# Kernel tuning notes

Hardware: AMD Instinct MI355X
Metric: run time of the kernel (lower is better)

The kernel has to match this reference:

```python
import jax, jax.numpy as jnp
import numpy as np

CIN, HID, OUT = 128, 256, 349
NTYPES, ETYPES = 4, 5
N0, N1, N2 = 120000, 40000, 10000
GNODES, GEDGES = 250000, 2000000
E0, E1 = 1500000, 400000


def setup_inputs() -> dict:
    key = jax.random.key(0)
    ks = jax.random.split(key, 24)
    ri = jax.random.randint
    rn = jax.random.normal
    inp = {}
    inp['n_id'] = ri(ks[0], (N0,), 0, GNODES)
    inp['x0'] = rn(ks[1], (100000, CIN), dtype=jnp.float32)
    inp['src0'] = ri(ks[2], (E0,), 0, N0)
    inp['dst0'] = ri(ks[3], (E0,), 0, N1)
    inp['e_id0'] = ri(ks[4], (E0,), 0, GEDGES)
    inp['src1'] = ri(ks[5], (E1,), 0, N1)
    inp['dst1'] = ri(ks[6], (E1,), 0, N2)
    inp['e_id1'] = ri(ks[7], (E1,), 0, GEDGES)
    inp['edge_type'] = ri(ks[8], (GEDGES,), 0, ETYPES)
    inp['node_type'] = ri(ks[9], (GNODES,), 0, NTYPES)
    inp['local_node_idx'] = ri(ks[10], (GNODES,), 0, 50000)
    # learned parameters
    inp['emb1'] = rn(ks[11], (50000, CIN), dtype=jnp.float32)
    inp['emb2'] = rn(ks[12], (50000, CIN), dtype=jnp.float32)
    inp['emb3'] = rn(ks[13], (50000, CIN), dtype=jnp.float32)
    s0 = 1.0 / np.sqrt(CIN)
    s1 = 1.0 / np.sqrt(HID)
    inp['relW0'] = rn(ks[14], (ETYPES, CIN, HID), dtype=jnp.float32) * s0
    inp['rootW0'] = rn(ks[15], (NTYPES, CIN, HID), dtype=jnp.float32) * s0
    inp['rootb0'] = rn(ks[16], (NTYPES, HID), dtype=jnp.float32) * 0.02
    inp['relW1'] = rn(ks[17], (ETYPES, HID, OUT), dtype=jnp.float32) * s1
    inp['rootW1'] = rn(ks[18], (NTYPES, HID, OUT), dtype=jnp.float32) * s1
    inp['rootb1'] = rn(ks[19], (NTYPES, OUT), dtype=jnp.float32) * 0.02
    return inp


def _group_input(tables, node_type, local_node_idx, n_id):
    # RGNN.group_input: per-node-type gather from feature / embedding tables.
    nt = node_type[n_id]            # [N0]
    li = local_node_idx[n_id]       # [N0]
    h = jnp.zeros((n_id.shape[0], CIN), dtype=tables[0].dtype)
    for k, tab in enumerate(tables):
        idx = jnp.minimum(li, tab.shape[0] - 1)
        h = jnp.where((nt == k)[:, None], tab[idx], h)
    return h, nt


def _rgcn_layer(x, nt_src, src, dst, et, relW, rootW, rootb, n_tgt):
    # out = sum_t mean-aggregate(x_j over edges of type t) @ W_t  (linear commutes with mean)
    T = relW.shape[0]
    xj = x[src]                                           # [E, Cin] gather
    seg = dst * T + et                                    # fused (target, edge_type) segment id
    sums = jax.ops.segment_sum(xj, seg, num_segments=n_tgt * T)
    cnts = jax.ops.segment_sum(jnp.ones((src.shape[0],), x.dtype), seg, num_segments=n_tgt * T)
    mean = (sums / jnp.maximum(cnts, 1.0)[:, None]).reshape(n_tgt, T, -1)  # [Nt, T, Cin]
    out = jnp.einsum('ntc,tco->no', mean, relW)           # [Nt, Cout]
    # per-node-type root linear: out[mask] += root_lins[i](x_target[mask])
    x_t = x[:n_tgt]
    nt_t = nt_src[:n_tgt]
    allr = jnp.einsum('nc,tco->tno', x_t, rootW) + rootb[:, None, :]  # [Tn, Nt, Cout]
    root = jnp.take_along_axis(allr, nt_t[None, :, None], axis=0)[0]
    return out + root


def reference(n_id, x0, src0, dst0, e_id0, src1, dst1, e_id1, edge_type, node_type,
              local_node_idx, emb1, emb2, emb3, relW0, rootW0, rootb0, relW1, rootW1, rootb1):
    h, nt = _group_input([x0, emb1, emb2, emb3], node_type, local_node_idx, n_id)
    # layer 0: I -> H
    h = _rgcn_layer(h, nt, src0, dst0, edge_type[e_id0], relW0, rootW0, rootb0, N1)
    h = jax.nn.relu(h)
    nt = nt[:N1]
    # layer 1: H -> O
    h = _rgcn_layer(h, nt, src1, dst1, edge_type[e_id1], relW1, rootW1, rootb1, N2)
    return jax.nn.log_softmax(h, axis=-1)
```

## Files before the change

kernel.cpp:

```cpp
#include <hip/hip_runtime.h>
#include <hip/hip_bf16.h>
#include <cmath>

constexpr int kCIN = 128, kHID = 256, kOUT = 349;
constexpr int kNT = 4, kET = 5;
constexpr int kN0 = 120000, kN1 = 40000, kN2 = 10000;
constexpr int kNSEG0 = kN1 * kET;
constexpr int kNSEG1 = kN2 * kET;
constexpr int kNSEG = kNSEG0 + kNSEG1;

constexpr int kBinSegs = 512;
constexpr int kNBin0 = (kNSEG0 + kBinSegs - 1) / kBinSegs;
constexpr int kNBin1 = (kNSEG1 + kBinSegs - 1) / kBinSegs;
constexpr int kNBin  = kNBin0 + kNBin1;
constexpr int kNBLK  = 512;
constexpr int kSB    = 128;

typedef __bf16 bf16x8 __attribute__((ext_vector_type(8)));
typedef float f32x4 __attribute__((ext_vector_type(4)));
typedef float f32x2v __attribute__((ext_vector_type(2)));
typedef unsigned short ushort8v __attribute__((ext_vector_type(8)));

__device__ __forceinline__ unsigned short f2b(float f) {
    unsigned int b = __float_as_uint(f);
    unsigned int r = (b + 0x7FFFu + ((b >> 16) & 1u)) >> 16;
    return (unsigned short)r;
}
__device__ __forceinline__ float b2f(unsigned short u) {
    return __uint_as_float((unsigned int)u << 16);
}
__device__ __forceinline__ void gl2lds16(const void* g, void* l) {
    __builtin_amdgcn_global_load_lds(
        (const __attribute__((address_space(1))) void*)g,
        (__attribute__((address_space(3))) void*)l, 16, 0, 0);
}

__device__ __forceinline__ unsigned int f2e4m3(float f) {
#if __has_builtin(__builtin_amdgcn_cvt_pk_fp8_f32)
    return (unsigned int)(__builtin_amdgcn_cvt_pk_fp8_f32(f, f, 0, false) & 0xFF);
#else
    unsigned int sb = (__float_as_uint(f) >> 31) << 7;
    float m = fminf(fabsf(f), 448.f);
    unsigned int code;
    if (m < 0.015625f) {
        code = (unsigned int)__float2int_rn(m * 512.f);
    } else {
        unsigned int b = __float_as_uint(m);
        b = b + 0x7FFFF + ((b >> 20) & 1);
        int e8 = (int)(b >> 23) - 120;
        if (e8 > 15) code = 0x7E;
        else code = ((unsigned int)e8 << 3) | ((b >> 20) & 7);
    }
    return sb | code;
#endif
}

__device__ __forceinline__ void e4m3x4_to_f32(unsigned int u, float* o4) {
#if __has_builtin(__builtin_amdgcn_cvt_pk_f32_fp8)
    f32x2v a = __builtin_amdgcn_cvt_pk_f32_fp8(u, false);
    f32x2v b = __builtin_amdgcn_cvt_pk_f32_fp8(u, true);
    o4[0] = a[0]; o4[1] = a[1]; o4[2] = b[0]; o4[3] = b[1];
#else
#pragma unroll
    for (int i = 0; i < 4; i++) {
        unsigned int c = (u >> (8 * i)) & 0xFF;
        unsigned int s = c >> 7, e = (c >> 3) & 15, mm = c & 7;
        float v;
        if (e == 0) v = (float)mm * 0.001953125f;
        else        v = __uint_as_float((e + 120u) << 23 | mm << 20);
        o4[i] = s ? -v : v;
    }
#endif
}

__global__ void k_prep(const float* __restrict__ relW0, const float* __restrict__ rootW0,
                       unsigned short* __restrict__ Bt0T,
                       const float* __restrict__ relW1, const float* __restrict__ rootW1,
                       unsigned short* __restrict__ Bt1T,
                       const int* __restrict__ etype, unsigned char* __restrict__ et8, int nET)
{
    constexpr int T0 = kNT * 256 * 768;
    constexpr int T1 = kNT * 384 * 1536;
    constexpr int TP = T0 + T1;
    int i = blockIdx.x * 256 + threadIdx.x;
    if (i < T0) {
        int g = i / (256 * 768);
        int rem = i - g * (256 * 768);
        int col = rem / 768;
        int k = rem - col * 768;
        float v = (k < 640) ? relW0[(size_t)k * 256 + col]
                            : rootW0[((size_t)g * 128 + (k - 640)) * 256 + col];
        Bt0T[i] = f2b(v);
    } else if (i < TP) {
        int ii = i - T0;
        int g = ii / (384 * 1536);
        int rem = ii - g * (384 * 1536);
        int col = rem / 1536;
        int k = rem - col * 1536;
        float v = 0.f;
        if (col < kOUT) v = (k < 1280) ? relW1[(size_t)k * kOUT + col]
                                       : rootW1[((size_t)g * 256 + (k - 1280)) * kOUT + col];
        Bt1T[ii] = f2b(v);
    } else {
        int k = i - TP;
        if (k < nET) et8[k] = (unsigned char)etype[k];
    }
}

__global__ void k_gather(const int* __restrict__ n_id, const float* __restrict__ x0,
                         const float* __restrict__ e1, const float* __restrict__ e2,
                         const float* __restrict__ e3, const int* __restrict__ ntype,
                         const int* __restrict__ lidx, unsigned short* __restrict__ h0b,
                         unsigned char* __restrict__ h0f8, int* __restrict__ nt0)
{
    int row = blockIdx.x * 8 + (threadIdx.x >> 5);
    if (row >= kN0) return;
    int lane = threadIdx.x & 31;
    int gid = n_id[row];
    int nt = ntype[gid];
    int li = lidx[gid];
    const float* tab;
    int rows;
    if (nt == 0)      { tab = x0; rows = 100000; }
    else if (nt == 1) { tab = e1; rows = 50000; }
    else if (nt == 2) { tab = e2; rows = 50000; }
    else              { tab = e3; rows = 50000; }
    int idx = li < rows ? li : rows - 1;
    float4 v = reinterpret_cast<const float4*>(tab + (size_t)idx * kCIN)[lane];
    ushort4 o;
    o.x = f2b(v.x); o.y = f2b(v.y); o.z = f2b(v.z); o.w = f2b(v.w);
    reinterpret_cast<ushort4*>(h0b + (size_t)row * kCIN)[lane] = o;
    unsigned int q = f2e4m3(v.x) | (f2e4m3(v.y) << 8) | (f2e4m3(v.z) << 16) | (f2e4m3(v.w) << 24);
    reinterpret_cast<unsigned int*>(h0f8 + (size_t)row * kCIN)[lane] = q;
    if (lane == 0) nt0[row] = nt;
}

__global__ __launch_bounds__(1024) void k_bincnt(
    const int* __restrict__ dst0, const int* __restrict__ eid0, int E0,
    const int* __restrict__ dst1, const int* __restrict__ eid1, int E1,
    const unsigned char* __restrict__ et8, int* __restrict__ cnts2d,
    int* __restrict__ seg32,
    const int* __restrict__ nt0, int* __restrict__ ntcnts)
{
    __shared__ int h[kNBin];
    const int tid = threadIdx.x;
    if (blockIdx.x < kNBLK) {
        for (int k = tid; k < kNBin; k += 1024) h[k] = 0;
        __syncthreads();
        int Etot = E0 + E1;
        int chunk = (Etot + kNBLK - 1) / kNBLK;
        int lo = blockIdx.x * chunk;
        int hi = min(lo + chunk, Etot);
        for (int i = lo + tid; i < hi; i += 1024) {
            int c;
            if (i < E0) c = dst0[i] * kET + (int)et8[eid0[i]];
            else { int e = i - E0; c = kNBin0 * kBinSegs + dst1[e] * kET + (int)et8[eid1[e]]; }
            seg32[i] = c;
            atomicAdd(&h[c >> 9], 1);
        }
        __syncthreads();
        for (int k = tid; k < kNBin; k += 1024) cnts2d[(size_t)k * kNBLK + blockIdx.x] = h[k];
    } else {
        int b = blockIdx.x - kNBLK;
        int layer = b >= kSB;
        int blk = b - layer * kSB;
        int M = layer ? kN2 : kN1;
        if (tid < 4) h[tid] = 0;
        __syncthreads();
        int chunk = (M + kSB - 1) / kSB;
        int lo = blk * chunk, hi = min(lo + chunk, M);
        for (int i = lo + tid; i < hi; i += 1024) atomicAdd(&h[nt0[i]], 1);
        __syncthreads();
        if (tid < 4) ntcnts[(layer * 4 + tid) * kSB + blk] = h[tid];
    }
}

__global__ void k_scan1(const int* __restrict__ cnt, int* __restrict__ excl,
                        int* __restrict__ blksum, int n)
{
    __shared__ int sm[1024];
    int i = blockIdx.x * 1024 + threadIdx.x;
    int v = (i < n) ? cnt[i] : 0;
    sm[threadIdx.x] = v;
    __syncthreads();
    for (int off = 1; off < 1024; off <<= 1) {
        int t = (threadIdx.x >= off) ? sm[threadIdx.x - off] : 0;
        __syncthreads();
        sm[threadIdx.x] += t;
        __syncthreads();
    }
    if (i < n) excl[i] = sm[threadIdx.x] - v;
    if (threadIdx.x == 1023) blksum[blockIdx.x] = sm[1023];
}

__global__ __launch_bounds__(1024) void k_scan2(
    int* __restrict__ blksum, int nblk,
    const int* __restrict__ ntcnts, int* __restrict__ ntoffs,
    int* __restrict__ goff0, int* __restrict__ goff1)
{
    __shared__ int sm[1024];
    int tid = threadIdx.x;
    if (blockIdx.x == 0) {
        int v = (tid < nblk) ? blksum[tid] : 0;
        sm[tid] = v;
        __syncthreads();
        for (int off = 1; off < 1024; off <<= 1) {
            int t = (tid >= off) ? sm[tid - off] : 0;
            __syncthreads();
            sm[tid] += t;
            __syncthreads();
        }
        if (tid < nblk) blksum[tid] = sm[tid] - v;
    } else {
        int v = ntcnts[tid];
        sm[tid] = v;
        __syncthreads();
        for (int off = 1; off < 512; off <<= 1) {
            int t = 0;
            if ((tid & 511) >= off) t = sm[tid - off];
            __syncthreads();
            sm[tid] += t;
            __syncthreads();
        }
        int excl = sm[tid] - v;
        ntoffs[tid] = excl;
        if ((tid & 127) == 0) {
            int layer = tid >> 9;
            int t = (tid >> 7) & 3;
            if (layer == 0) goff0[t] = excl; else goff1[t] = excl;
        }
        if (tid == 0) { goff0[4] = kN1; goff1[4] = kN2; }
    }
}

__global__ __launch_bounds__(1024) void k_binplace(
    const int* __restrict__ src0, int E0,
    const int* __restrict__ src1, int E1,
    const int* __restrict__ seg32,
    const int* __restrict__ offs2d, const int* __restrict__ blksum,
    unsigned int* __restrict__ pairs,
    const int* __restrict__ nt0, const int* __restrict__ ntoffs,
    int* __restrict__ perm0, int* __restrict__ perm1)
{
    __shared__ int cur[kNBin];
    const int tid = threadIdx.x;
    if (blockIdx.x < kNBLK) {
        for (int k = tid; k < kNBin; k += 1024) {
            size_t li = (size_t)k * kNBLK + blockIdx.x;
            cur[k] = offs2d[li] + blksum[li >> 10];
        }
        __syncthreads();
        int Etot = E0 + E1;
        int chunk = (Etot + kNBLK - 1) / kNBLK;
        int lo = blockIdx.x * chunk;
        int hi = min(lo + chunk, Etot);
        for (int i = lo + tid; i < hi; i += 1024) {
            int c = seg32[i];
            int s = (i < E0) ? src0[i] : src1[i - E0];
            unsigned int pay = (unsigned int)s | ((unsigned int)(c & (kBinSegs - 1)) << 17);
            int p = atomicAdd(&cur[c >> 9], 1);
            pairs[p] = pay;
        }
    } else {
        int b = blockIdx.x - kNBLK;
        int layer = b >= kSB;
        int blk = b - layer * kSB;
        int M = layer ? kN2 : kN1;
        int* perm = layer ? perm1 : perm0;
        if (tid < 4) cur[tid] = ntoffs[(layer * 4 + tid) * kSB + blk];
        __syncthreads();
        int chunk = (M + kSB - 1) / kSB;
        int lo = blk * chunk, hi = min(lo + chunk, M);
        for (int i = lo + tid; i < hi; i += 1024) {
            int p = atomicAdd(&cur[nt0[i]], 1);
            perm[p] = i;
        }
    }
}

__global__ __launch_bounds__(1024) void k_binscatter(
    const int* __restrict__ offs2d, const int* __restrict__ blksum, int Etot,
    const unsigned int* __restrict__ pairs,
    int* __restrict__ order, int* __restrict__ starts, int* __restrict__ cnt)
{
    __shared__ int h[kBinSegs];
    __shared__ int sc[kBinSegs];
    __shared__ int cur[kBinSegs];
    const int bin = blockIdx.x;
    const int tid = threadIdx.x;
    size_t bi = (size_t)bin * kNBLK;
    const int base = offs2d[bi] + blksum[bi >> 10];
    int end = Etot;
    if (bin + 1 < kNBin) {
        size_t ei = (size_t)(bin + 1) * kNBLK;
        end = offs2d[ei] + blksum[ei >> 10];
    }
    const int c = end - base;
    const unsigned int* pp = pairs + base;

    for (int k = tid; k < kBinSegs; k += 1024) h[k] = 0;
    __syncthreads();
    for (int j = tid; j < c; j += 1024) atomicAdd(&h[pp[j] >> 17], 1);
    __syncthreads();
    if (tid < kBinSegs) sc[tid] = h[tid];
    __syncthreads();
    for (int off = 1; off < kBinSegs; off <<= 1) {
        int t = 0;
        if (tid < kBinSegs && tid >= off) t = sc[tid - off];
        __syncthreads();
        if (tid < kBinSegs) sc[tid] += t;
        __syncthreads();
    }
    int seg_rel, abs_base, seglim;
    if (bin < kNBin0) { seg_rel = bin * kBinSegs; abs_base = seg_rel; seglim = kNSEG0 - seg_rel; }
    else { seg_rel = (bin - kNBin0) * kBinSegs; abs_base = kNSEG0 + seg_rel; seglim = kNSEG1 - seg_rel; }
    if (tid < kBinSegs) {
        int excl = sc[tid] - h[tid];
        cur[tid] = excl;
        if (tid < seglim) {
            starts[abs_base + tid] = base + excl;
            cnt[abs_base + tid] = h[tid];
        }
    }
    __syncthreads();
    for (int j = tid; j < c; j += 1024) {
        unsigned int u = pp[j];
        int sl = (int)(u >> 17);
        int p = atomicAdd(&cur[sl], 1);
        order[base + p] = (int)(u & 0x1FFFFu);
    }
}

template<int C>
__global__ __launch_bounds__(256) void k_segreduce8(
    const int* __restrict__ starts, const int* __restrict__ cnt,
    const int* __restrict__ order, const unsigned char* __restrict__ h8,
    unsigned short* __restrict__ mean, int nseg)
{
    constexpr int L = C / 16;
    constexpr int SPB = 256 / L;
    int sidx = blockIdx.x * SPB + threadIdx.x / L;
    if (sidx >= nseg) return;
    int lane = threadIdx.x % L;
    int st = starts[sidx];
    int n = cnt[sidx];
    const unsigned char* hp = h8 + (size_t)lane * 16;
    float a0[16], a1[16];
#pragma unroll
    for (int i = 0; i < 16; i++) { a0[i] = 0.f; a1[i] = 0.f; }
    int j = 0;
    for (; j + 2 <= n; j += 2) {
        int s0 = order[st + j + 0];
        int s1 = order[st + j + 1];
        uint4 u0 = *reinterpret_cast<const uint4*>(hp + (size_t)s0 * C);
        uint4 u1 = *reinterpret_cast<const uint4*>(hp + (size_t)s1 * C);
        float d[16];
        e4m3x4_to_f32(u0.x, d); e4m3x4_to_f32(u0.y, d + 4);
        e4m3x4_to_f32(u0.z, d + 8); e4m3x4_to_f32(u0.w, d + 12);
#pragma unroll
        for (int i = 0; i < 16; i++) a0[i] += d[i];
        e4m3x4_to_f32(u1.x, d); e4m3x4_to_f32(u1.y, d + 4);
        e4m3x4_to_f32(u1.z, d + 8); e4m3x4_to_f32(u1.w, d + 12);
#pragma unroll
        for (int i = 0; i < 16; i++) a1[i] += d[i];
    }
    if (j < n) {
        int s0 = order[st + j];
        uint4 u0 = *reinterpret_cast<const uint4*>(hp + (size_t)s0 * C);
        float d[16];
        e4m3x4_to_f32(u0.x, d); e4m3x4_to_f32(u0.y, d + 4);
        e4m3x4_to_f32(u0.z, d + 8); e4m3x4_to_f32(u0.w, d + 12);
#pragma unroll
        for (int i = 0; i < 16; i++) a0[i] += d[i];
    }
    float sc = 1.0f / fmaxf((float)n, 1.0f);
    ushort8v o0, o1;
#pragma unroll
    for (int i = 0; i < 8; i++) {
        o0[i] = f2b((a0[i] + a1[i]) * sc);
        o1[i] = f2b((a0[i + 8] + a1[i + 8]) * sc);
    }
    unsigned short* mp = mean + (size_t)sidx * C + lane * 16;
    *reinterpret_cast<ushort8v*>(mp) = o0;
    *reinterpret_cast<ushort8v*>(mp + 8) = o1;
}

template<int C, int BM, int BNF, int NCB, int WR, int WC, int RELU, int OUTBF16, int OUTF8>
__global__ __launch_bounds__(256) void k_gemm_sorted(
    int M, int Nreal, int NpadK,
    const unsigned short* __restrict__ meanb,
    const unsigned short* __restrict__ hb,
    const unsigned short* __restrict__ BtT,
    const float* __restrict__ rootb,
    const int* __restrict__ perm, const int* __restrict__ goff,
    unsigned short* __restrict__ outb, float* __restrict__ outf,
    unsigned char* __restrict__ outf8)
{
    constexpr int K1 = kET * C;
    constexpr int K  = K1 + C;
    constexpr int FM = BM / (16 * WR);
    constexpr int FN = BNF / (16 * WC);
    __shared__ __align__(16) char ldsA[BM * 128];
    __shared__ __align__(16) char ldsB[BNF * 128];

    int nwg = gridDim.x;
    int orig = blockIdx.x;
    int q = nwg >> 3, r8 = nwg & 7, x8 = orig & 7;
    int logical = (x8 < r8 ? x8 * (q + 1) : r8 * (q + 1) + (x8 - r8) * q) + (orig >> 3);
    int colb = logical % NCB;
    int t = logical / NCB;

    int g, row0s = 0, gend = 0;
    {
        int gs[5] = {goff[0], goff[1], goff[2], goff[3], goff[4]};
        int tb = 0;
        for (g = 0; g < 4; ++g) {
            int cg = gs[g + 1] - gs[g];
            int ntl = (cg + BM - 1) / BM;
            if (t < tb + ntl) { row0s = gs[g] + (t - tb) * BM; gend = gs[g + 1]; break; }
            tb += ntl;
        }
        if (g == 4) return;
    }
    const int rows_here = min(BM, gend - row0s);
    const unsigned short* BtG = BtT + (size_t)g * NpadK;

    const int tid = threadIdx.x;
    const int col0 = colb * BNF;
    const int wid = tid >> 6, lane = tid & 63;
    const int wrow = (wid / WC) * (BM / WR);
    const int wcol = (wid % WC) * (BNF / WC);
    const int lr = lane >> 3;
    const int kb = (lane & 7) * 16;

    f32x4 acc[FM][FN] = {};

    for (int k0 = 0; k0 < K; k0 += 64) {
        const bool inMean = (k0 < K1);
        const size_t kB = (size_t)k0 * 2;
#pragma unroll
        for (int c2 = 0; c2 < BM / 32; ++c2) {
            int rb = (wid * (BM / 32) + c2) * 8;
            int r = rb + lr;
            int pr = perm[row0s + min(r, rows_here - 1)];
            const char* rowp = inMean
                ? (const char*)(meanb + (size_t)pr * K1) + kB
                : (const char*)(hb + (size_t)pr * C) + (kB - (size_t)K1 * 2);
            gl2lds16(rowp + (kb ^ ((r & 7) << 4)), &ldsA[rb * 128]);
        }
#pragma unroll
        for (int c2 = 0; c2 < BNF / 32; ++c2) {
            int rb = (wid * (BNF / 32) + c2) * 8;
            int r = rb + lr;
            const char* rowp = (const char*)(BtG + (size_t)(col0 + r) * K) + kB;
            gl2lds16(rowp + (kb ^ ((r & 7) << 4)), &ldsB[rb * 128]);
        }
        __syncthreads();
#pragma unroll
        for (int kc = 0; kc < 2; kc++) {
            int kb2 = kc * 64 + (lane >> 4) * 16;
            bf16x8 af[FM], bfr[FN];
#pragma unroll
            for (int m = 0; m < FM; m++) {
                int r = wrow + m * 16 + (lane & 15);
                af[m] = *reinterpret_cast<const bf16x8*>(&ldsA[r * 128 + (kb2 ^ ((r & 7) << 4))]);
            }
#pragma unroll
            for (int n = 0; n < FN; n++) {
                int r = wcol + n * 16 + (lane & 15);
                bfr[n] = *reinterpret_cast<const bf16x8*>(&ldsB[r * 128 + (kb2 ^ ((r & 7) << 4))]);
            }
#pragma unroll
            for (int m = 0; m < FM; m++)
#pragma unroll
                for (int n = 0; n < FN; n++)
                    acc[m][n] = __builtin_amdgcn_mfma_f32_16x16x32_bf16(af[m], bfr[n], acc[m][n], 0, 0, 0);
        }
        __syncthreads();
    }

#pragma unroll
    for (int m = 0; m < FM; m++) {
        int rlb = wrow + m * 16 + (lane >> 4) * 4;
#pragma unroll
        for (int n = 0; n < FN; n++) {
            int col = col0 + wcol + n * 16 + (lane & 15);
            if (col >= Nreal) continue;
            f32x4 v = acc[m][n];
#pragma unroll
            for (int j = 0; j < 4; j++) {
                int rl = rlb + j;
                if (rl >= rows_here) continue;
                int orig_row = perm[row0s + rl];
                float xv = v[j] + rootb[g * Nreal + col];
                if (RELU) xv = fmaxf(xv, 0.f);
                if (OUTBF16) {
                    outb[(size_t)orig_row * Nreal + col] = f2b(xv);
                    if (OUTF8) outf8[(size_t)orig_row * Nreal + col] = (unsigned char)f2e4m3(xv);
                } else {
                    outf[(size_t)orig_row * Nreal + col] = xv;
                }
            }
        }
    }
}

__global__ void k_logsm(float* __restrict__ out, int M, int N)
{
    int row = blockIdx.x * 4 + (threadIdx.x >> 6);
    if (row >= M) return;
    int lane = threadIdx.x & 63;
    float* p = out + (size_t)row * N;
    float mx = -3.4e38f;
    for (int c = lane; c < N; c += 64) mx = fmaxf(mx, p[c]);
#pragma unroll
    for (int o = 32; o > 0; o >>= 1) mx = fmaxf(mx, __shfl_xor(mx, o));
    float s = 0.f;
    for (int c = lane; c < N; c += 64) s += expf(p[c] - mx);
#pragma unroll
    for (int o = 32; o > 0; o >>= 1) s += __shfl_xor(s, o);
    float lse = mx + logf(s);
    for (int c = lane; c < N; c += 64) p[c] -= lse;
}

extern "C" void kernel_launch(void* const* d_in, const int* in_sizes, int n_in,
                              void* d_out, int out_size, void* d_ws, size_t ws_size,
                              hipStream_t stream)
{
    const int*   n_id   = (const int*)d_in[0];
    const float* x0     = (const float*)d_in[1];
    const int*   src0   = (const int*)d_in[2];
    const int*   dst0   = (const int*)d_in[3];
    const int*   eid0   = (const int*)d_in[4];
    const int*   src1   = (const int*)d_in[5];
    const int*   dst1   = (const int*)d_in[6];
    const int*   eid1   = (const int*)d_in[7];
    const int*   etype  = (const int*)d_in[8];
    const int*   ntype  = (const int*)d_in[9];
    const int*   lidx   = (const int*)d_in[10];
    const float* emb1   = (const float*)d_in[11];
    const float* emb2   = (const float*)d_in[12];
    const float* emb3   = (const float*)d_in[13];
    const float* relW0  = (const float*)d_in[14];
    const float* rootW0 = (const float*)d_in[15];
    const float* rootb0 = (const float*)d_in[16];
    const float* relW1  = (const float*)d_in[17];
    const float* rootW1 = (const float*)d_in[18];
    const float* rootb1 = (const float*)d_in[19];
    float* out = (float*)d_out;

    const int E0 = in_sizes[2];
    const int E1 = in_sizes[5];
    const int Etot = E0 + E1;
    const int nET = in_sizes[8];
    constexpr int K0s  = kET * kCIN + kCIN;
    constexpr int K1s  = kET * kHID + kHID;
    constexpr int Npad0 = 256;
    constexpr int Npad1 = 384;

    char* ws = (char*)d_ws;
    size_t off = 0;
    auto alloc = [&](size_t bytes) -> void* {
        void* p = ws + off;
        off = (off + bytes + 255) & ~(size_t)255;
        return p;
    };
    unsigned short* h0b   = (unsigned short*)alloc((size_t)kN0 * kCIN * 2);
    unsigned char*  h0f8  = (unsigned char*)alloc((size_t)kN0 * kCIN);
    int*            nt0   = (int*)alloc((size_t)kN0 * 4);
    unsigned short* meanb = (unsigned short*)alloc((size_t)kNSEG0 * kCIN * 2);
    int*            cnt    = (int*)alloc((size_t)kNSEG * 4);
    int*            starts = (int*)alloc((size_t)kNSEG * 4);
    int*            cnts2d = (int*)alloc((size_t)kNBin * kNBLK * 4);
    int*            offs2d = (int*)alloc((size_t)kNBin * kNBLK * 4);
    int*            blksum = (int*)alloc(1024 * 4);
    unsigned int*   pairs  = (unsigned int*)alloc((size_t)Etot * 4);
    int*            order  = (int*)alloc((size_t)Etot * 4);
    int*            seg32  = (int*)alloc((size_t)Etot * 4);
    unsigned char*  et8    = (unsigned char*)alloc((size_t)nET);
    unsigned short* h1b   = (unsigned short*)alloc((size_t)kN1 * kHID * 2);
    unsigned char*  h1f8  = (unsigned char*)alloc((size_t)kN1 * kHID);
    unsigned short* Bt0T  = (unsigned short*)alloc((size_t)kNT * Npad0 * K0s * 2);
    unsigned short* Bt1T  = (unsigned short*)alloc((size_t)kNT * Npad1 * K1s * 2);
    int*            perm0  = (int*)alloc((size_t)kN1 * 4);
    int*            goff0  = (int*)alloc(8 * 4);
    int*            perm1  = (int*)alloc((size_t)kN2 * 4);
    int*            goff1  = (int*)alloc(8 * 4);
    int*            ntcnts = (int*)alloc(1024 * 4);
    int*            ntoffs = (int*)alloc(1024 * 4);

    constexpr int TPREP = kNT * Npad0 * K0s + kNT * Npad1 * K1s;
    int prep_total = TPREP + nET;
    k_prep<<<(prep_total + 255) / 256, 256, 0, stream>>>(relW0, rootW0, Bt0T, relW1, rootW1, Bt1T,
                                                         etype, et8, nET);
    k_gather<<<(kN0 + 7) / 8, 256, 0, stream>>>(n_id, x0, emb1, emb2, emb3, ntype, lidx, h0b, h0f8, nt0);

    k_bincnt<<<kNBLK + 2 * kSB, 1024, 0, stream>>>(dst0, eid0, E0, dst1, eid1, E1, et8,
                                                   cnts2d, seg32, nt0, ntcnts);
    int nscan = kNBin * kNBLK;
    int nblk = (nscan + 1023) / 1024;
    k_scan1<<<nblk, 1024, 0, stream>>>(cnts2d, offs2d, blksum, nscan);
    k_scan2<<<2, 1024, 0, stream>>>(blksum, nblk, ntcnts, ntoffs, goff0, goff1);
    k_binplace<<<kNBLK + 2 * kSB, 1024, 0, stream>>>(src0, E0, src1, E1, seg32,
                                                     offs2d, blksum, pairs, nt0, ntoffs, perm0, perm1);
    k_binscatter<<<kNBin, 1024, 0, stream>>>(offs2d, blksum, Etot, pairs, order, starts, cnt);

    k_segreduce8<kCIN><<<(kNSEG0 + 31) / 32, 256, 0, stream>>>(starts, cnt, order, h0f8, meanb, kNSEG0);
    int g0 = kN1 / 64 + 4;
    k_gemm_sorted<kCIN, 64, 256, 1, 2, 2, 1, 1, 1><<<g0, 256, 0, stream>>>(
        kN1, kHID, Npad0 * K0s, meanb, h0b, Bt0T, rootb0, perm0, goff0, h1b, nullptr, h1f8);

    k_segreduce8<kHID><<<(kNSEG1 + 15) / 16, 256, 0, stream>>>(starts + kNSEG0, cnt + kNSEG0, order, h1f8, meanb, kNSEG1);
    int g1 = (kN2 / 64 + 5) * 3;
    k_gemm_sorted<kHID, 64, 128, 3, 2, 2, 0, 0, 0><<<g1, 256, 0, stream>>>(
        kN2, kOUT, Npad1 * K1s, meanb, h1b, Bt1T, rootb1, perm1, goff1, nullptr, out, nullptr);

    k_logsm<<<(kN2 + 3) / 4, 256, 0, stream>>>(out, kN2, kOUT);
}
```

Baseline: 260.9 us.

## Fuse input gather into bin-count kernel and split layer-0 GEMM N tiles

The separate feature-gather kernel is folded into the bin-count launch as extra blocks, so gather and edge counting run concurrently in one launch. The node-type histogram now reads ntype[n_id[i]] directly instead of depending on nt0 written by the gather. Separately, the layer-0 GEMM tile width drops from 256 to 128 columns with twice as many blocks, for more parallelism at the cost of re-reading the A operand. The gather now runs in 1024-thread blocks that share the kernel's static shared-memory histogram, which may reduce occupancy for those blocks.

```diff
diff --git a/kernel.cpp b/kernel.cpp
--- a/kernel.cpp
+++ b/kernel.cpp
@@ -15,6 +15,7 @@
 constexpr int kNBin  = kNBin0 + kNBin1;
 constexpr int kNBLK  = 512;
 constexpr int kSB    = 128;
+constexpr int kGB    = (kN0 + 31) / 32;
 
 typedef __bf16 bf16x8 __attribute__((ext_vector_type(8)));
 typedef float f32x4 __attribute__((ext_vector_type(4)));
@@ -107,40 +108,17 @@
     }
 }
 
-__global__ void k_gather(const int* __restrict__ n_id, const float* __restrict__ x0,
-                         const float* __restrict__ e1, const float* __restrict__ e2,
-                         const float* __restrict__ e3, const int* __restrict__ ntype,
-                         const int* __restrict__ lidx, unsigned short* __restrict__ h0b,
-                         unsigned char* __restrict__ h0f8, int* __restrict__ nt0)
-{
-    int row = blockIdx.x * 8 + (threadIdx.x >> 5);
-    if (row >= kN0) return;
-    int lane = threadIdx.x & 31;
-    int gid = n_id[row];
-    int nt = ntype[gid];
-    int li = lidx[gid];
-    const float* tab;
-    int rows;
-    if (nt == 0)      { tab = x0; rows = 100000; }
-    else if (nt == 1) { tab = e1; rows = 50000; }
-    else if (nt == 2) { tab = e2; rows = 50000; }
-    else              { tab = e3; rows = 50000; }
-    int idx = li < rows ? li : rows - 1;
-    float4 v = reinterpret_cast<const float4*>(tab + (size_t)idx * kCIN)[lane];
-    ushort4 o;
-    o.x = f2b(v.x); o.y = f2b(v.y); o.z = f2b(v.z); o.w = f2b(v.w);
-    reinterpret_cast<ushort4*>(h0b + (size_t)row * kCIN)[lane] = o;
-    unsigned int q = f2e4m3(v.x) | (f2e4m3(v.y) << 8) | (f2e4m3(v.z) << 16) | (f2e4m3(v.w) << 24);
-    reinterpret_cast<unsigned int*>(h0f8 + (size_t)row * kCIN)[lane] = q;
-    if (lane == 0) nt0[row] = nt;
-}
-
 __global__ __launch_bounds__(1024) void k_bincnt(
     const int* __restrict__ dst0, const int* __restrict__ eid0, int E0,
     const int* __restrict__ dst1, const int* __restrict__ eid1, int E1,
     const unsigned char* __restrict__ et8, int* __restrict__ cnts2d,
     int* __restrict__ seg32,
-    const int* __restrict__ nt0, int* __restrict__ ntcnts)
+    const int* __restrict__ n_id, const int* __restrict__ ntype, int* __restrict__ ntcnts,
+    const float* __restrict__ x0, const float* __restrict__ e1f,
+    const float* __restrict__ e2f, const float* __restrict__ e3f,
+    const int* __restrict__ lidx,
+    unsigned short* __restrict__ h0b, unsigned char* __restrict__ h0f8,
+    int* __restrict__ nt0)
 {
     __shared__ int h[kNBin];
     const int tid = threadIdx.x;
@@ -160,7 +138,7 @@
         }
         __syncthreads();
         for (int k = tid; k < kNBin; k += 1024) cnts2d[(size_t)k * kNBLK + blockIdx.x] = h[k];
-    } else {
+    } else if (blockIdx.x < kNBLK + 2 * kSB) {
         int b = blockIdx.x - kNBLK;
         int layer = b >= kSB;
         int blk = b - layer * kSB;
@@ -169,9 +147,30 @@
         __syncthreads();
         int chunk = (M + kSB - 1) / kSB;
         int lo = blk * chunk, hi = min(lo + chunk, M);
-        for (int i = lo + tid; i < hi; i += 1024) atomicAdd(&h[nt0[i]], 1);
+        for (int i = lo + tid; i < hi; i += 1024) atomicAdd(&h[ntype[n_id[i]]], 1);
         __syncthreads();
         if (tid < 4) ntcnts[(layer * 4 + tid) * kSB + blk] = h[tid];
+    } else {
+        int row = (blockIdx.x - kNBLK - 2 * kSB) * 32 + (tid >> 5);
+        if (row >= kN0) return;
+        int lane = tid & 31;
+        int gid = n_id[row];
+        int nt = ntype[gid];
+        int li = lidx[gid];
+        const float* tab;
+        int rows;
+        if (nt == 0)      { tab = x0;  rows = 100000; }
+        else if (nt == 1) { tab = e1f; rows = 50000; }
+        else if (nt == 2) { tab = e2f; rows = 50000; }
+        else              { tab = e3f; rows = 50000; }
+        int idx = li < rows ? li : rows - 1;
+        float4 v = reinterpret_cast<const float4*>(tab + (size_t)idx * kCIN)[lane];
+        ushort4 o;
+        o.x = f2b(v.x); o.y = f2b(v.y); o.z = f2b(v.z); o.w = f2b(v.w);
+        reinterpret_cast<ushort4*>(h0b + (size_t)row * kCIN)[lane] = o;
+        unsigned int q = f2e4m3(v.x) | (f2e4m3(v.y) << 8) | (f2e4m3(v.z) << 16) | (f2e4m3(v.w) << 24);
+        reinterpret_cast<unsigned int*>(h0f8 + (size_t)row * kCIN)[lane] = q;
+        if (lane == 0) nt0[row] = nt;
     }
 }
 
@@ -593,10 +592,11 @@
     int prep_total = TPREP + nET;
     k_prep<<<(prep_total + 255) / 256, 256, 0, stream>>>(relW0, rootW0, Bt0T, relW1, rootW1, Bt1T,
                                                          etype, et8, nET);
-    k_gather<<<(kN0 + 7) / 8, 256, 0, stream>>>(n_id, x0, emb1, emb2, emb3, ntype, lidx, h0b, h0f8, nt0);
-
-    k_bincnt<<<kNBLK + 2 * kSB, 1024, 0, stream>>>(dst0, eid0, E0, dst1, eid1, E1, et8,
-                                                   cnts2d, seg32, nt0, ntcnts);
+
+    k_bincnt<<<kNBLK + 2 * kSB + kGB, 1024, 0, stream>>>(
+        dst0, eid0, E0, dst1, eid1, E1, et8, cnts2d, seg32,
+        n_id, ntype, ntcnts, x0, emb1, emb2, emb3, lidx, h0b, h0f8, nt0);
+
     int nscan = kNBin * kNBLK;
     int nblk = (nscan + 1023) / 1024;
     k_scan1<<<nblk, 1024, 0, stream>>>(cnts2d, offs2d, blksum, nscan);
@@ -606,8 +606,8 @@
     k_binscatter<<<kNBin, 1024, 0, stream>>>(offs2d, blksum, Etot, pairs, order, starts, cnt);
 
     k_segreduce8<kCIN><<<(kNSEG0 + 31) / 32, 256, 0, stream>>>(starts, cnt, order, h0f8, meanb, kNSEG0);
-    int g0 = kN1 / 64 + 4;
-    k_gemm_sorted<kCIN, 64, 256, 1, 2, 2, 1, 1, 1><<<g0, 256, 0, stream>>>(
+    int g0 = (kN1 / 64 + 4) * 2;
+    k_gemm_sorted<kCIN, 64, 128, 2, 2, 2, 1, 1, 1><<<g0, 256, 0, stream>>>(
         kN1, kHID, Npad0 * K0s, meanb, h0b, Bt0T, rootb0, perm0, goff0, h1b, nullptr, h1f8);
 
     k_segreduce8<kHID><<<(kNSEG1 + 15) / 16, 256, 0, stream>>>(starts + kNSEG0, cnt + kNSEG0, order, h1f8, meanb, kNSEG1);
```

Result: faster. 236.3 us (-9.4%).
